# Kernel optimization log

Hardware: AMD Instinct MI355X
Metric: run time of the kernel (lower is better)

The kernel has to match this reference:

```python
import jax, jax.numpy as jnp
import numpy as np

B, A, T, D, H, NB, OUT = 64, 128, 6, 256, 512, 5, 401
ALPHA = 0.5
BETA = 0.5


def _lin_init(key, n_in, n_out, extra=()):
    bound = 1.0 / np.sqrt(n_in)
    kw, kb = jax.random.split(key)
    W = jax.random.uniform(kw, extra + (n_in, n_out), minval=-bound, maxval=bound, dtype=jnp.float32)
    b = jax.random.uniform(kb, extra + (n_out,), minval=-bound, maxval=bound, dtype=jnp.float32)
    return W, b


def setup_inputs() -> dict:
    key = jax.random.key(0)
    ks = jax.random.split(key, 8)
    stdv = 1.0 / np.sqrt(D)
    anchor = jax.random.uniform(ks[0], (1, 1, T, D), minval=-stdv, maxval=stdv, dtype=jnp.float32)
    sW1, sb1 = _lin_init(ks[1], D, D, (NB,))
    sW2, sb2 = _lin_init(ks[2], D, D, (NB,))
    cW1, cb1 = _lin_init(ks[3], D, D, (NB,))
    cW2, cb2 = _lin_init(ks[4], D, D, (NB,))
    dW1, db1 = _lin_init(ks[5], D, H)
    dW2, db2 = _lin_init(ks[6], H, OUT)
    final_embedding = jax.random.normal(ks[7], (B, A, D), dtype=jnp.float32)
    return {"final_embedding": final_embedding, "anchor": anchor,
            "sW1": sW1, "sb1": sb1, "sW2": sW2, "sb2": sb2,
            "cW1": cW1, "cb1": cb1, "cW2": cW2, "cb2": cb2,
            "dW1": dW1, "db1": db1, "dW2": dW2, "db2": db2}


def _mlp2(x, W1, b1, W2, b2):
    # 2-layer MLP (Linear -> ReLU -> Linear), applied to last dim
    return jax.nn.relu(x @ W1 + b1) @ W2 + b2


def reference(final_embedding, anchor, sW1, sb1, sW2, sb2, cW1, cb1, cW2, cb2, dW1, db1, dW2, db2):
    b, a = final_embedding.shape[:2]
    # s: [B, A, T, D] repeated anchors; c: [B, A, 1, D] context
    s = jnp.broadcast_to(anchor, (b, a, T, D))
    c = final_embedding[:, :, None, :]
    for i in range(NB):
        s_new = _mlp2(s, sW1[i], sb1[i], sW2[i], sb2[i])
        c_new = _mlp2(c, cW1[i], cb1[i], cW2[i], cb2[i])
        s_new = s_new * c_new                      # gate, broadcasts over T
        agg_c = jnp.max(s_new, axis=-2, keepdims=True)
        s = ALPHA * s + BETA * s_new               # sliding running mean
        c = ALPHA * c + BETA * agg_c
    # decoder MLP on trajectory embeddings s: [B, A, T, D]
    res = jax.nn.relu(s @ dW1 + db1) @ dW2 + db2   # [B, A, T, 401]
    coordinates = res[..., :160].reshape(b, a, T, 80, 2)
    av = res[..., 160:240].reshape(b, a, T, 80, 1)
    bv = res[..., 240:320].reshape(b, a, T, 80, 1)
    cv = res[..., 320:400].reshape(b, a, T, 80, 1)
    probas = res[..., -1]                          # [B, A, T]
    cov = jnp.concatenate([jnp.exp(av) * jnp.cosh(bv), jnp.sinh(bv),
                           jnp.sinh(bv), jnp.exp(-av) * jnp.cosh(bv)], axis=-1) * jnp.exp(cv)
    covariance_matrices = cov.reshape(b, a, T, 80, 2, 2)
    return (probas, coordinates, covariance_matrices)
```

## Files before the change

kernel.cpp:

```cpp
#include <hip/hip_runtime.h>
#include <math.h>


constexpr int Tn  = 6;
constexpr int Dn  = 256;
constexpr int Hn  = 512;
constexpr int NBn = 5;
constexpr int OUTn = 401;
constexpr int BA  = 8192;
constexpr int MR  = 49152;
constexpr float kAlpha = 0.5f;
constexpr float kBeta  = 0.5f;

typedef __bf16 bf16_8 __attribute__((ext_vector_type(8)));
typedef float  f32x4  __attribute__((ext_vector_type(4)));

__device__ __forceinline__ void async_copy16(const __bf16* g, __bf16* l) {
  __builtin_amdgcn_global_load_lds(
      (const __attribute__((address_space(1))) void*)g,
      (__attribute__((address_space(3))) void*)l, 16, 0, 0);
}

template<bool RELU, bool OUT_BF16>
__global__ __launch_bounds__(256) void gemm_mfma(
    const __bf16* __restrict__ A, const __bf16* __restrict__ BT,
    const float* __restrict__ bias, void* __restrict__ Cout,
    int M, int N, int K)
{
  __shared__ __align__(16) char smem[34816];

  const int tid = threadIdx.x;
  const int l   = tid & 63;
  const int w   = tid >> 6;
  const int wm  = w >> 1, wn = w & 1;

  const int GX = gridDim.x;
  const int total = GX * gridDim.y;
  const int L = blockIdx.y * GX + blockIdx.x;
  const int xcd = L & 7, pos = L >> 3;
  const int base = total >> 3, rem = total & 7;
  const int start = xcd * base + (xcd < rem ? xcd : rem);
  const int TL = start + pos;
  const int my = TL / GX;
  const int nx = TL - my * GX;
  const int m0 = my * 128;
  const int n0 = nx * 128;

  const int lrow = l >> 2;
  const int lk   = (l & 3) * 8;
  int ar0 = m0 + w * 32 + lrow;        if (ar0 > M - 1) ar0 = M - 1;
  int ar1 = m0 + w * 32 + 16 + lrow;   if (ar1 > M - 1) ar1 = M - 1;
  int br0 = n0 + w * 32 + lrow;        if (br0 > N - 1) br0 = N - 1;
  int br1 = n0 + w * 32 + 16 + lrow;   if (br1 > N - 1) br1 = N - 1;
  const __bf16* Ag0 = A  + (size_t)ar0 * K + lk;
  const __bf16* Ag1 = A  + (size_t)ar1 * K + lk;
  const __bf16* Bg0 = BT + (size_t)br0 * K + lk;
  const __bf16* Bg1 = BT + (size_t)br1 * K + lk;

  f32x4 acc[4][4];
#pragma unroll
  for (int i = 0; i < 4; ++i)
#pragma unroll
    for (int j = 0; j < 4; ++j) acc[i][j] = (f32x4){0.f, 0.f, 0.f, 0.f};

  auto stage = [&](int buf, int ko) {
    __bf16* As = (__bf16*)(smem + buf * 16384);
    __bf16* Bs = As + 4096;
    async_copy16(Ag0 + ko, As + w * 1024);
    async_copy16(Ag1 + ko, As + w * 1024 + 512);
    async_copy16(Bg0 + ko, Bs + w * 1024);
    async_copy16(Bg1 + ko, Bs + w * 1024 + 512);
  };

  const int kIters = K >> 5;
  stage(0, 0);
  __syncthreads();
  for (int kt = 0; kt < kIters; ++kt) {
    if (kt + 1 < kIters) stage((kt + 1) & 1, (kt + 1) * 32);
    const __bf16* As = (const __bf16*)(smem + (kt & 1) * 16384);
    const __bf16* Bs = As + 4096;
    const __bf16* ap = As + (wm * 64 + (l & 15)) * 32 + (l >> 4) * 8;
    const __bf16* bp = Bs + (wn * 64 + (l & 15)) * 32 + (l >> 4) * 8;

    bf16_8 af[4], bf[4];
#pragma unroll
    for (int i = 0; i < 4; ++i) af[i] = *(const bf16_8*)(ap + i * 16 * 32);
#pragma unroll
    for (int j = 0; j < 4; ++j) bf[j] = *(const bf16_8*)(bp + j * 16 * 32);
#pragma unroll
    for (int i = 0; i < 4; ++i)
#pragma unroll
      for (int j = 0; j < 4; ++j)
        acc[i][j] = __builtin_amdgcn_mfma_f32_16x16x32_bf16(af[i], bf[j], acc[i][j], 0, 0, 0);
    __syncthreads();
  }

  const int colb = n0 + wn * 64 + (l & 15);
  const int rowb = m0 + wm * 64 + (l >> 4) * 4;

  if (OUT_BF16) {
    __bf16* Cs = (__bf16*)smem;
    const int lrb = wm * 64 + (l >> 4) * 4;
    const int lcb = wn * 64 + (l & 15);
#pragma unroll
    for (int j = 0; j < 4; ++j) {
      const float bj = bias[colb + j * 16];
#pragma unroll
      for (int i = 0; i < 4; ++i) {
#pragma unroll
        for (int r = 0; r < 4; ++r) {
          float v = acc[i][j][r] + bj;
          if (RELU) v = fmaxf(v, 0.0f);
          Cs[(lrb + i * 16 + r) * 136 + lcb + j * 16] = (__bf16)v;
        }
      }
    }
    __syncthreads();
    __bf16* Cg = (__bf16*)Cout;
#pragma unroll
    for (int it = 0; it < 8; ++it) {
      const int idx = it * 256 + tid;
      const int row = idx >> 4, c16 = idx & 15;
      const int gr = m0 + row;
      if (gr < M) {
        uint4 v = *(const uint4*)(Cs + row * 136 + c16 * 8);
        *(uint4*)(Cg + (size_t)gr * N + n0 + c16 * 8) = v;
      }
    }
  } else {
#pragma unroll
    for (int j = 0; j < 4; ++j) {
      const int gc = colb + j * 16;
      if (gc >= N) continue;
      const float bj = bias[gc];
#pragma unroll
      for (int i = 0; i < 4; ++i) {
        const int gr0 = rowb + i * 16;
#pragma unroll
        for (int r = 0; r < 4; ++r) {
          const int gr = gr0 + r;
          if (gr >= M) continue;
          float v = acc[i][j][r] + bj;
          if (RELU) v = fmaxf(v, 0.0f);
          ((float*)Cout)[(size_t)gr * N + gc] = v;
        }
      }
    }
  }
}

__global__ __launch_bounds__(512) void mlp2_c(
    const __bf16* __restrict__ X, const __bf16* __restrict__ W1T,
    const float* __restrict__ b1, const __bf16* __restrict__ W2T,
    const float* __restrict__ b2, __bf16* __restrict__ Out)
{
  __shared__ __align__(16) char smem[53248];
  __bf16* Hb = (__bf16*)(smem + 36864);

  const int tid = threadIdx.x, l = tid & 63, w = tid >> 6;
  const int m0 = blockIdx.x * 32;
  const int q4 = (l >> 4) * 4;

  f32x4 acc[2][2];
#pragma unroll
  for (int i = 0; i < 2; ++i)
#pragma unroll
    for (int j = 0; j < 2; ++j) acc[i][j] = (f32x4){0.f, 0.f, 0.f, 0.f};

  const __bf16* Xg = X + (size_t)(m0 + (tid >> 2)) * Dn + (tid & 3) * 8;

  auto stageA = [&](int buf, int kt) {
    if (tid < 128)
      async_copy16(Xg + kt * 32, (__bf16*)(smem + buf * 2048) + tid * 8);
  };
  auto stageW = [&](const __bf16* WT, int buf, int kt) {
    __bf16* Wstb = (__bf16*)(smem + 4096 + buf * 16384);
#pragma unroll
    for (int r2 = 0; r2 < 2; ++r2) {
      const int ch = tid + r2 * 512, row = ch >> 2, kk = (ch & 3) * 8;
      async_copy16(WT + (size_t)row * Dn + kt * 32 + kk, Wstb + ch * 8);
    }
  };

  stageA(0, 0); stageW(W1T, 0, 0);
  __syncthreads();
  for (int kt = 0; kt < 8; ++kt) {
    if (kt < 7) { stageA((kt + 1) & 1, kt + 1); stageW(W1T, (kt + 1) & 1, kt + 1); }
    const __bf16* Astb = (const __bf16*)(smem + (kt & 1) * 2048);
    const __bf16* Wstb = (const __bf16*)(smem + 4096 + (kt & 1) * 16384);
    bf16_8 bf[2];
#pragma unroll
    for (int j = 0; j < 2; ++j)
      bf[j] = *(const bf16_8*)(Wstb + (w * 32 + j * 16 + (l & 15)) * 32 + (l >> 4) * 8);
#pragma unroll
    for (int i = 0; i < 2; ++i) {
      bf16_8 af = *(const bf16_8*)(Astb + (i * 16 + (l & 15)) * 32 + (l >> 4) * 8);
#pragma unroll
      for (int j = 0; j < 2; ++j)
        acc[i][j] = __builtin_amdgcn_mfma_f32_16x16x32_bf16(af, bf[j], acc[i][j], 0, 0, 0);
    }
    __syncthreads();
  }

#pragma unroll
  for (int j = 0; j < 2; ++j) {
    const int col = w * 32 + j * 16 + (l & 15);
    const float bj = b1[col];
    __bf16* hc = Hb + (col >> 5) * 1024 + (col & 31);
#pragma unroll
    for (int i = 0; i < 2; ++i)
#pragma unroll
      for (int r = 0; r < 4; ++r) {
        const int row = i * 16 + q4 + r;
        hc[row * 32] = (__bf16)fmaxf(acc[i][j][r] + bj, 0.0f);
      }
  }
  __syncthreads();

#pragma unroll
  for (int i = 0; i < 2; ++i)
#pragma unroll
    for (int j = 0; j < 2; ++j) acc[i][j] = (f32x4){0.f, 0.f, 0.f, 0.f};
  stageW(W2T, 0, 0);
  __syncthreads();
  for (int kt = 0; kt < 8; ++kt) {
    if (kt < 7) stageW(W2T, (kt + 1) & 1, kt + 1);
    const __bf16* Wstb = (const __bf16*)(smem + 4096 + (kt & 1) * 16384);
    bf16_8 bf[2];
#pragma unroll
    for (int j = 0; j < 2; ++j)
      bf[j] = *(const bf16_8*)(Wstb + (w * 32 + j * 16 + (l & 15)) * 32 + (l >> 4) * 8);
#pragma unroll
    for (int i = 0; i < 2; ++i) {
      bf16_8 af = *(const bf16_8*)(Hb + kt * 1024 + (i * 16 + (l & 15)) * 32 + (l >> 4) * 8);
#pragma unroll
      for (int j = 0; j < 2; ++j)
        acc[i][j] = __builtin_amdgcn_mfma_f32_16x16x32_bf16(af, bf[j], acc[i][j], 0, 0, 0);
    }
    __syncthreads();
  }

#pragma unroll
  for (int j = 0; j < 2; ++j) {
    const int col = w * 32 + j * 16 + (l & 15);
    const float bj = b2[col];
#pragma unroll
    for (int i = 0; i < 2; ++i)
#pragma unroll
      for (int r = 0; r < 4; ++r) {
        const int row = i * 16 + q4 + r;
        Out[(size_t)(m0 + row) * Dn + col] = (__bf16)(acc[i][j][r] + bj);
      }
  }
}

__global__ __launch_bounds__(512) void mlp2_s(
    __bf16* __restrict__ S, const __bf16* __restrict__ W1T,
    const float* __restrict__ b1, const __bf16* __restrict__ W2T,
    const float* __restrict__ b2, const __bf16* __restrict__ Cnew,
    __bf16* __restrict__ C)
{
  __shared__ __align__(16) char smem[71680];
  __bf16* Hb   = (__bf16*)(smem + 22528);
  __bf16* Snew = (__bf16*)smem;

  const int tid = threadIdx.x, l = tid & 63, w = tid >> 6;
  const int m0 = blockIdx.x * 96;
  const int q4 = (l >> 4) * 4;

  f32x4 acc[6][2];
#pragma unroll
  for (int i = 0; i < 6; ++i)
#pragma unroll
    for (int j = 0; j < 2; ++j) acc[i][j] = (f32x4){0.f, 0.f, 0.f, 0.f};

  const __bf16* Sg = S + (size_t)(m0 + (tid >> 2)) * Dn + (tid & 3) * 8;

  auto stageL1 = [&](int buf, int kt) {
    __bf16* Astb = (__bf16*)(smem + buf * 22528);
    __bf16* Wstb = (__bf16*)(smem + buf * 22528 + 6144);
    if (tid < 384) async_copy16(Sg + kt * 32, Astb + tid * 8);
#pragma unroll
    for (int r2 = 0; r2 < 2; ++r2) {
      const int ch = tid + r2 * 512, row = ch >> 2, kk = (ch & 3) * 8;
      async_copy16(W1T + (size_t)row * Dn + kt * 32 + kk, Wstb + ch * 8);
    }
  };

  stageL1(0, 0);
  __syncthreads();
  for (int kt = 0; kt < 8; ++kt) {
    if (kt < 7) stageL1((kt + 1) & 1, kt + 1);
    const __bf16* Astb = (const __bf16*)(smem + (kt & 1) * 22528);
    const __bf16* Wstb = Astb + 3072;
    bf16_8 bf[2];
#pragma unroll
    for (int j = 0; j < 2; ++j)
      bf[j] = *(const bf16_8*)(Wstb + (w * 32 + j * 16 + (l & 15)) * 32 + (l >> 4) * 8);
#pragma unroll
    for (int i = 0; i < 6; ++i) {
      bf16_8 af = *(const bf16_8*)(Astb + (i * 16 + (l & 15)) * 32 + (l >> 4) * 8);
#pragma unroll
      for (int j = 0; j < 2; ++j)
        acc[i][j] = __builtin_amdgcn_mfma_f32_16x16x32_bf16(af, bf[j], acc[i][j], 0, 0, 0);
    }
    __syncthreads();
  }

#pragma unroll
  for (int j = 0; j < 2; ++j) {
    const int col = w * 32 + j * 16 + (l & 15);
    const float bj = b1[col];
    __bf16* hc = Hb + (col >> 5) * (96 * 32) + (col & 31);
#pragma unroll
    for (int i = 0; i < 6; ++i)
#pragma unroll
      for (int r = 0; r < 4; ++r) {
        const int row = i * 16 + q4 + r;
        hc[row * 32] = (__bf16)fmaxf(acc[i][j][r] + bj, 0.0f);
      }
  }
  __syncthreads();

#pragma unroll
  for (int i = 0; i < 6; ++i)
#pragma unroll
    for (int j = 0; j < 2; ++j) acc[i][j] = (f32x4){0.f, 0.f, 0.f, 0.f};
  __bf16* Wst = (__bf16*)(smem + 6144);
  for (int kt = 0; kt < 8; ++kt) {
#pragma unroll
    for (int r2 = 0; r2 < 2; ++r2) {
      const int ch = tid + r2 * 512, row = ch >> 2, kk = (ch & 3) * 8;
      async_copy16(W2T + (size_t)row * Dn + kt * 32 + kk, Wst + ch * 8);
    }
    __syncthreads();
    bf16_8 bf[2];
#pragma unroll
    for (int j = 0; j < 2; ++j)
      bf[j] = *(const bf16_8*)(Wst + (w * 32 + j * 16 + (l & 15)) * 32 + (l >> 4) * 8);
#pragma unroll
    for (int i = 0; i < 6; ++i) {
      bf16_8 af = *(const bf16_8*)(Hb + kt * (96 * 32) + (i * 16 + (l & 15)) * 32 + (l >> 4) * 8);
#pragma unroll
      for (int j = 0; j < 2; ++j)
        acc[i][j] = __builtin_amdgcn_mfma_f32_16x16x32_bf16(af, bf[j], acc[i][j], 0, 0, 0);
    }
    __syncthreads();
  }

#pragma unroll
  for (int j = 0; j < 2; ++j) {
    const int col = w * 32 + j * 16 + (l & 15);
    const float bj = b2[col];
#pragma unroll
    for (int i = 0; i < 6; ++i)
#pragma unroll
      for (int r = 0; r < 4; ++r) {
        const int row = i * 16 + q4 + r;
        Snew[row * 264 + col] = (__bf16)(acc[i][j][r] + bj);
      }
  }
  __syncthreads();

  {
    const int ba = tid >> 5, dg = (tid & 31) * 8;
    const size_t gb = (size_t)(blockIdx.x * 16 + ba) * Dn + dg;
    bf16_8 cn8 = *(const bf16_8*)(Cnew + gb);
    float cn[8], m[8];
#pragma unroll
    for (int e = 0; e < 8; ++e) { cn[e] = (float)cn8[e]; m[e] = -3.402823466e38f; }
#pragma unroll
    for (int t = 0; t < Tn; ++t) {
      const int row = ba * 6 + t;
      bf16_8 sn8 = *(const bf16_8*)(Snew + row * 264 + dg);
      const size_t gs = (size_t)(m0 + row) * Dn + dg;
      bf16_8 s8 = *(const bf16_8*)(S + gs);
      bf16_8 o8;
#pragma unroll
      for (int e = 0; e < 8; ++e) {
        const float sn = (float)sn8[e] * cn[e];
        m[e] = fmaxf(m[e], sn);
        o8[e] = (__bf16)(kAlpha * (float)s8[e] + kBeta * sn);
      }
      *(bf16_8*)(S + gs) = o8;
    }
    bf16_8 c8 = *(const bf16_8*)(C + gb);
#pragma unroll
    for (int e = 0; e < 8; ++e)
      c8[e] = (__bf16)(kAlpha * (float)c8[e] + kBeta * m[e]);
    *(bf16_8*)(C + gb) = c8;
  }
}

__global__ __launch_bounds__(512, 4) void decoder2_fused(
    const __bf16* __restrict__ A, const __bf16* __restrict__ BT,
    const float* __restrict__ bias, float* __restrict__ out)
{
  __shared__ __align__(16) char smem[73728];
  float* mid = (float*)smem;

  const int tid = threadIdx.x, l = tid & 63, w = tid >> 6;
  const int m0 = blockIdx.x * 64;
  const int q4 = (l >> 4) * 4;

  f32x4 acc[4][4];
#pragma unroll
  for (int i = 0; i < 4; ++i)
#pragma unroll
    for (int j = 0; j < 4; ++j) acc[i][j] = (f32x4){0.f, 0.f, 0.f, 0.f};

  const __bf16* Ag = A + (size_t)(m0 + (tid >> 2)) * Hn + (tid & 3) * 8;
  const __bf16* Bg[4];
#pragma unroll
  for (int r4 = 0; r4 < 4; ++r4) {
    const int ch = tid + r4 * 512;
    int row = ch >> 2; if (row > 400) row = 400;
    Bg[r4] = BT + (size_t)row * Hn + (ch & 3) * 8;
  }

  auto stage = [&](int buf, int kt) {
    const int ko = kt * 32;
    __bf16* base = (__bf16*)(smem + buf * 36864);
    if (tid < 256) async_copy16(Ag + ko, base + tid * 8);
    __bf16* Bl = base + 64 * 32;
#pragma unroll
    for (int r4 = 0; r4 < 4; ++r4)
      async_copy16(Bg[r4] + ko, Bl + (size_t)(tid + r4 * 512) * 8);
  };

  stage(0, 0);
  __syncthreads();
  int cur = 0;
  for (int kt = 0; kt < 16; ++kt) {
    if (kt < 15) stage(cur ^ 1, kt + 1);
    const __bf16* Asl = (const __bf16*)(smem + cur * 36864);
    const __bf16* Bsl = Asl + 64 * 32;
    bf16_8 af[4], bf[4];
#pragma unroll
    for (int j = 0; j < 4; ++j)
      bf[j] = *(const bf16_8*)(Bsl + (w * 64 + j * 16 + (l & 15)) * 32 + (l >> 4) * 8);
#pragma unroll
    for (int i = 0; i < 4; ++i)
      af[i] = *(const bf16_8*)(Asl + (i * 16 + (l & 15)) * 32 + (l >> 4) * 8);
#pragma unroll
    for (int i = 0; i < 4; ++i)
#pragma unroll
      for (int j = 0; j < 4; ++j)
        acc[i][j] = __builtin_amdgcn_mfma_f32_16x16x32_bf16(af[i], bf[j], acc[i][j], 0, 0, 0);
    __syncthreads();
    cur ^= 1;
  }

  float* cov = out + MR + (size_t)MR * 160;
  const int gc = w * 64 + (l & 15);
#pragma unroll
  for (int sub = 0; sub < 2; ++sub) {
#pragma unroll
    for (int ih = 0; ih < 2; ++ih) {
      const int i = sub * 2 + ih;
#pragma unroll
      for (int j = 0; j < 4; ++j) {
        const int c = gc + j * 16;
        if (c > 400) continue;
        const float bj = bias[c];
#pragma unroll
        for (int r = 0; r < 4; ++r) {
          const int lr = ih * 16 + q4 + r;
          const int gr = m0 + sub * 32 + lr;
          const float v = acc[i][j][r] + bj;
          if (c < 160)      out[(size_t)MR + (size_t)gr * 160 + c] = v;
          else if (c < 400) mid[lr * 241 + (c - 160)] = v;
          else              out[gr] = v;
        }
      }
    }
    __syncthreads();
#pragma unroll
    for (int p = 0; p < 5; ++p) {
      const int q = p * 512 + tid;
      const int r32 = q / 80, j = q - r32 * 80;
      const int gr = m0 + sub * 32 + r32;
      const float av = mid[r32 * 241 + j];
      const float bv = mid[r32 * 241 + 80 + j];
      const float cv = mid[r32 * 241 + 160 + j];
      const float eb = __expf(bv), ebn = __expf(-bv);
      const float sh = 0.5f * (eb - ebn), ch = 0.5f * (eb + ebn);
      const float ea = __expf(av), ean = __expf(-av), ec = __expf(cv);
      f32x4 c4 = { ea * ch * ec, sh * ec, sh * ec, ean * ch * ec };
      *(f32x4*)(cov + (size_t)gr * 320 + 4 * j) = c4;
    }
    if (sub == 0) __syncthreads();
  }
}

__global__ __launch_bounds__(256) void transpose_bf16(
    const float* __restrict__ W, __bf16* __restrict__ WT, int K, int N)
{
  __shared__ float t[32][33];
  const int b  = blockIdx.z;
  const int tx = threadIdx.x, ty = threadIdx.y;
  const int k0 = blockIdx.y * 32, n0 = blockIdx.x * 32;
  const float* Wb  = W  + (size_t)b * K * N;
  __bf16*      WTb = WT + (size_t)b * N * K;
#pragma unroll
  for (int r = 0; r < 4; ++r) {
    int kk = k0 + ty + r * 8;
    if (kk < K && n0 + tx < N) t[ty + r * 8][tx] = Wb[(size_t)kk * N + n0 + tx];
  }
  __syncthreads();
#pragma unroll
  for (int r = 0; r < 4; ++r) {
    int nn = n0 + ty + r * 8;
    if (nn < N && k0 + tx < K)
      WTb[(size_t)nn * K + k0 + tx] = (__bf16)t[tx][ty + r * 8];
  }
}

__global__ __launch_bounds__(256) void convert_bf16(
    const float* __restrict__ in, __bf16* __restrict__ out, int n)
{
  int i = blockIdx.x * 256 + threadIdx.x;
  if (i < n) out[i] = (__bf16)in[i];
}

__global__ __launch_bounds__(256) void ew_update0(
    const float* __restrict__ anchor, const float* __restrict__ fe,
    const float* __restrict__ snewsm, const __bf16* __restrict__ cnew,
    __bf16* __restrict__ s, __bf16* __restrict__ c)
{
  int q = blockIdx.x * 256 + threadIdx.x;
  if (q >= BA * 32) return;
  int ba = q >> 5;
  int dg = (q & 31) * 8;
  bf16_8 cn8 = *(const bf16_8*)(cnew + (size_t)ba * Dn + dg);
  float cn[8], m[8];
#pragma unroll
  for (int e = 0; e < 8; ++e) { cn[e] = (float)cn8[e]; m[e] = -3.402823466e38f; }
  size_t base = (size_t)ba * Tn * Dn + dg;
#pragma unroll
  for (int t = 0; t < Tn; ++t) {
    bf16_8 o8;
#pragma unroll
    for (int e = 0; e < 8; ++e) {
      float sn = snewsm[t * Dn + dg + e] * cn[e];
      m[e] = fmaxf(m[e], sn);
      o8[e] = (__bf16)(kAlpha * anchor[t * Dn + dg + e] + kBeta * sn);
    }
    *(bf16_8*)(s + base + t * Dn) = o8;
  }
  bf16_8 c8;
#pragma unroll
  for (int e = 0; e < 8; ++e)
    c8[e] = (__bf16)(kAlpha * fe[(size_t)ba * Dn + dg + e] + kBeta * m[e]);
  *(bf16_8*)(c + (size_t)ba * Dn + dg) = c8;
}

extern "C" void kernel_launch(void* const* d_in, const int* in_sizes, int n_in,
                              void* d_out, int out_size, void* d_ws, size_t ws_size,
                              hipStream_t stream) {
  const float* fe     = (const float*)d_in[0];
  const float* anchor = (const float*)d_in[1];
  const float* sW1 = (const float*)d_in[2];
  const float* sb1 = (const float*)d_in[3];
  const float* sW2 = (const float*)d_in[4];
  const float* sb2 = (const float*)d_in[5];
  const float* cW1 = (const float*)d_in[6];
  const float* cb1 = (const float*)d_in[7];
  const float* cW2 = (const float*)d_in[8];
  const float* cb2 = (const float*)d_in[9];
  const float* dW1 = (const float*)d_in[10];
  const float* db1 = (const float*)d_in[11];
  const float* dW2 = (const float*)d_in[12];
  const float* db2 = (const float*)d_in[13];
  float* out = (float*)d_out;

  char* p = (char*)d_ws;
  __bf16* s_bf    = (__bf16*)(p + 0);
  __bf16* hd_bf   = (__bf16*)(p + 25165824);
  __bf16* c_bf    = (__bf16*)(p + 75497472);
  __bf16* cnew_bf = (__bf16*)(p + 79691776);
  __bf16* fe_bf   = (__bf16*)(p + 83886080);
  __bf16* sWT1    = (__bf16*)(p + 88080384);
  __bf16* sWT2    = (__bf16*)(p + 88735744);
  __bf16* cWT1    = (__bf16*)(p + 89391104);
  __bf16* cWT2    = (__bf16*)(p + 90046464);
  __bf16* dWT1    = (__bf16*)(p + 90701824);
  __bf16* dWT2    = (__bf16*)(p + 90963968);
  __bf16* anc_bf  = (__bf16*)(p + 91374592);
  __bf16* hsm_bf  = (__bf16*)(p + 91377664);
  float*  snewsm_f= (float* )(p + 91380736);

  auto gemm = [&](const __bf16* A, const __bf16* BT, const float* b, void* C,
                  int M, int N, int K, bool relu, bool outbf) {
    dim3 grid((N + 127) / 128, (M + 127) / 128);
    if (relu) {
      if (outbf) gemm_mfma<true,  true ><<<grid, 256, 0, stream>>>(A, BT, b, C, M, N, K);
      else       gemm_mfma<true,  false><<<grid, 256, 0, stream>>>(A, BT, b, C, M, N, K);
    } else {
      if (outbf) gemm_mfma<false, true ><<<grid, 256, 0, stream>>>(A, BT, b, C, M, N, K);
      else       gemm_mfma<false, false><<<grid, 256, 0, stream>>>(A, BT, b, C, M, N, K);
    }
  };

  {
    dim3 blk(32, 8);
    dim3 g88(8, 8, NBn);
    transpose_bf16<<<g88, blk, 0, stream>>>(sW1, sWT1, Dn, Dn);
    transpose_bf16<<<g88, blk, 0, stream>>>(sW2, sWT2, Dn, Dn);
    transpose_bf16<<<g88, blk, 0, stream>>>(cW1, cWT1, Dn, Dn);
    transpose_bf16<<<g88, blk, 0, stream>>>(cW2, cWT2, Dn, Dn);
    transpose_bf16<<<dim3(16, 8, 1), blk, 0, stream>>>(dW1, dWT1, Dn, Hn);
    transpose_bf16<<<dim3(13, 16, 1), blk, 0, stream>>>(dW2, dWT2, Hn, OUTn);
  }
  convert_bf16<<<(BA * Dn + 255) / 256, 256, 0, stream>>>(fe, fe_bf, BA * Dn);
  convert_bf16<<<(Tn * Dn + 255) / 256, 256, 0, stream>>>(anchor, anc_bf, Tn * Dn);

  const size_t WKK = (size_t)Dn * Dn;

  gemm(anc_bf, sWT1, sb1, hsm_bf,   Tn, Dn, Dn, true,  true);
  gemm(hsm_bf, sWT2, sb2, snewsm_f, Tn, Dn, Dn, false, false);
  mlp2_c<<<BA / 32, 512, 0, stream>>>(fe_bf, cWT1, cb1, cWT2, cb2, cnew_bf);
  ew_update0<<<(BA * 32 + 255) / 256, 256, 0, stream>>>(anchor, fe, snewsm_f,
                                                        cnew_bf, s_bf, c_bf);

  for (int i = 1; i < NBn; ++i) {
    mlp2_c<<<BA / 32, 512, 0, stream>>>(c_bf, cWT1 + i * WKK, cb1 + i * Dn,
                                        cWT2 + i * WKK, cb2 + i * Dn, cnew_bf);
    mlp2_s<<<MR / 96, 512, 0, stream>>>(s_bf, sWT1 + i * WKK, sb1 + i * Dn,
                                        sWT2 + i * WKK, sb2 + i * Dn,
                                        cnew_bf, c_bf);
  }

  gemm(s_bf, dWT1, db1, hd_bf, MR, Hn, Dn, true, true);
  decoder2_fused<<<MR / 64, 512, 0, stream>>>(hd_bf, dWT2, db2, out);
}
```

Measured before the change: 393.4 us.

## Fuse context MLP into trajectory MLP kernel per block

Merges the separate mlp2_c launch into mlp2_s, so each block first computes the context MLP for its own 16 agent rows and keeps the result in shared memory. This removes one kernel launch per block iteration and the global round trip for c_new. In exchange, each block does a serial 16-row MLP with poor MFMA utilisation (one A tile per step) before its main work, which lengthens the critical path inside each block.

Result: faster. 374.4 us (-4.8%).

```diff
diff --git a/kernel.cpp b/kernel.cpp
--- a/kernel.cpp
+++ b/kernel.cpp
@@ -254,19 +254,108 @@
   }
 }
 
-__global__ __launch_bounds__(512) void mlp2_s(
-    __bf16* __restrict__ S, const __bf16* __restrict__ W1T,
-    const float* __restrict__ b1, const __bf16* __restrict__ W2T,
-    const float* __restrict__ b2, const __bf16* __restrict__ Cnew,
+__global__ __launch_bounds__(512) void mlp2_cs(
+    __bf16* __restrict__ S,
+    const __bf16* __restrict__ sW1T, const float* __restrict__ sb1,
+    const __bf16* __restrict__ sW2T, const float* __restrict__ sb2,
+    const __bf16* __restrict__ cW1T, const float* __restrict__ cb1,
+    const __bf16* __restrict__ cW2T, const float* __restrict__ cb2,
     __bf16* __restrict__ C)
 {
   __shared__ __align__(16) char smem[71680];
-  __bf16* Hb   = (__bf16*)(smem + 22528);
-  __bf16* Snew = (__bf16*)smem;
+  __bf16* Hb    = (__bf16*)(smem + 22528);
+  __bf16* Snew  = (__bf16*)smem;
+  __bf16* Hc    = (__bf16*)(smem + 45056);
+  __bf16* CnewL = (__bf16*)(smem + 53248);
 
   const int tid = threadIdx.x, l = tid & 63, w = tid >> 6;
-  const int m0 = blockIdx.x * 96;
-  const int q4 = (l >> 4) * 4;
+  const int m0  = blockIdx.x * 96;
+  const int ba0 = blockIdx.x * 16;
+  const int q4  = (l >> 4) * 4;
+
+  {
+    f32x4 ac[2];
+    ac[0] = (f32x4){0.f, 0.f, 0.f, 0.f};
+    ac[1] = (f32x4){0.f, 0.f, 0.f, 0.f};
+
+    const __bf16* Cg = C + (size_t)(ba0 + (tid >> 2)) * Dn + (tid & 3) * 8;
+
+    auto stageC1 = [&](int buf, int kt) {
+      __bf16* Astb = (__bf16*)(smem + buf * 22528);
+      __bf16* Wstb = Astb + 3072;
+      if (tid < 64) async_copy16(Cg + kt * 32, Astb + tid * 8);
+#pragma unroll
+      for (int r2 = 0; r2 < 2; ++r2) {
+        const int ch = tid + r2 * 512, row = ch >> 2, kk = (ch & 3) * 8;
+        async_copy16(cW1T + (size_t)row * Dn + kt * 32 + kk, Wstb + ch * 8);
+      }
+    };
+    stageC1(0, 0);
+    __syncthreads();
+    for (int kt = 0; kt < 8; ++kt) {
+      if (kt < 7) stageC1((kt + 1) & 1, kt + 1);
+      const __bf16* Astb = (const __bf16*)(smem + (kt & 1) * 22528);
+      const __bf16* Wstb = Astb + 3072;
+      bf16_8 bf[2];
+#pragma unroll
+      for (int j = 0; j < 2; ++j)
+        bf[j] = *(const bf16_8*)(Wstb + (w * 32 + j * 16 + (l & 15)) * 32 + (l >> 4) * 8);
+      bf16_8 af = *(const bf16_8*)(Astb + (l & 15) * 32 + (l >> 4) * 8);
+#pragma unroll
+      for (int j = 0; j < 2; ++j)
+        ac[j] = __builtin_amdgcn_mfma_f32_16x16x32_bf16(af, bf[j], ac[j], 0, 0, 0);
+      __syncthreads();
+    }
+
+#pragma unroll
+    for (int j = 0; j < 2; ++j) {
+      const int col = w * 32 + j * 16 + (l & 15);
+      const float bj = cb1[col];
+      __bf16* hc = Hc + (col >> 5) * 512 + (col & 31);
+#pragma unroll
+      for (int r = 0; r < 4; ++r)
+        hc[(q4 + r) * 32] = (__bf16)fmaxf(ac[j][r] + bj, 0.0f);
+    }
+    __syncthreads();
+
+    ac[0] = (f32x4){0.f, 0.f, 0.f, 0.f};
+    ac[1] = (f32x4){0.f, 0.f, 0.f, 0.f};
+    auto stageC2 = [&](int buf, int kt) {
+      __bf16* Wstb = (__bf16*)(smem + buf * 22528 + 6144);
+#pragma unroll
+      for (int r2 = 0; r2 < 2; ++r2) {
+        const int ch = tid + r2 * 512, row = ch >> 2, kk = (ch & 3) * 8;
+        async_copy16(cW2T + (size_t)row * Dn + kt * 32 + kk, Wstb + ch * 8);
+      }
+    };
+    stageC2(0, 0);
+    __syncthreads();
+    for (int kt = 0; kt < 8; ++kt) {
+      if (kt < 7) stageC2((kt + 1) & 1, kt + 1);
+      const __bf16* Wstb = (const __bf16*)(smem + (kt & 1) * 22528 + 6144);
+      bf16_8 bf[2];
+#pragma unroll
+      for (int j = 0; j < 2; ++j)
+        bf[j] = *(const bf16_8*)(Wstb + (w * 32 + j * 16 + (l & 15)) * 32 + (l >> 4) * 8);
+      bf16_8 af = *(const bf16_8*)(Hc + kt * 512 + (l & 15) * 32 + (l >> 4) * 8);
+#pragma unroll
+      for (int j = 0; j < 2; ++j)
+        ac[j] = __builtin_amdgcn_mfma_f32_16x16x32_bf16(af, bf[j], ac[j], 0, 0, 0);
+      __syncthreads();
+    }
+
+#pragma unroll
+    for (int j = 0; j < 2; ++j) {
+      const int col = w * 32 + j * 16 + (l & 15);
+      const float bj = cb2[col];
+#pragma unroll
+      for (int r = 0; r < 4; ++r)
+        CnewL[(q4 + r) * 264 + col] = (__bf16)(ac[j][r] + bj);
+    }
+    __syncthreads();
+  }
+
+  bf16_8 cn8 = *(const bf16_8*)(CnewL + (tid >> 5) * 264 + (tid & 31) * 8);
 
   f32x4 acc[6][2];
 #pragma unroll
@@ -283,7 +372,7 @@
 #pragma unroll
     for (int r2 = 0; r2 < 2; ++r2) {
       const int ch = tid + r2 * 512, row = ch >> 2, kk = (ch & 3) * 8;
-      async_copy16(W1T + (size_t)row * Dn + kt * 32 + kk, Wstb + ch * 8);
+      async_copy16(sW1T + (size_t)row * Dn + kt * 32 + kk, Wstb + ch * 8);
     }
   };
 
@@ -310,7 +399,7 @@
 #pragma unroll
   for (int j = 0; j < 2; ++j) {
     const int col = w * 32 + j * 16 + (l & 15);
-    const float bj = b1[col];
+    const float bj = sb1[col];
     __bf16* hc = Hb + (col >> 5) * (96 * 32) + (col & 31);
 #pragma unroll
     for (int i = 0; i < 6; ++i)
@@ -331,7 +420,7 @@
 #pragma unroll
     for (int r2 = 0; r2 < 2; ++r2) {
       const int ch = tid + r2 * 512, row = ch >> 2, kk = (ch & 3) * 8;
-      async_copy16(W2T + (size_t)row * Dn + kt * 32 + kk, Wst + ch * 8);
+      async_copy16(sW2T + (size_t)row * Dn + kt * 32 + kk, Wst + ch * 8);
     }
     __syncthreads();
     bf16_8 bf[2];
@@ -351,7 +440,7 @@
 #pragma unroll
   for (int j = 0; j < 2; ++j) {
     const int col = w * 32 + j * 16 + (l & 15);
-    const float bj = b2[col];
+    const float bj = sb2[col];
 #pragma unroll
     for (int i = 0; i < 6; ++i)
 #pragma unroll
@@ -364,8 +453,7 @@
 
   {
     const int ba = tid >> 5, dg = (tid & 31) * 8;
-    const size_t gb = (size_t)(blockIdx.x * 16 + ba) * Dn + dg;
-    bf16_8 cn8 = *(const bf16_8*)(Cnew + gb);
+    const size_t gb = (size_t)(ba0 + ba) * Dn + dg;
     float cn[8], m[8];
 #pragma unroll
     for (int e = 0; e < 8; ++e) { cn[e] = (float)cn8[e]; m[e] = -3.402823466e38f; }
@@ -624,11 +712,11 @@
                                                         cnew_bf, s_bf, c_bf);
 
   for (int i = 1; i < NBn; ++i) {
-    mlp2_c<<<BA / 32, 512, 0, stream>>>(c_bf, cWT1 + i * WKK, cb1 + i * Dn,
-                                        cWT2 + i * WKK, cb2 + i * Dn, cnew_bf);
-    mlp2_s<<<MR / 96, 512, 0, stream>>>(s_bf, sWT1 + i * WKK, sb1 + i * Dn,
-                                        sWT2 + i * WKK, sb2 + i * Dn,
-                                        cnew_bf, c_bf);
+    mlp2_cs<<<MR / 96, 512, 0, stream>>>(
+        s_bf,
+        sWT1 + i * WKK, sb1 + i * Dn, sWT2 + i * WKK, sb2 + i * Dn,
+        cWT1 + i * WKK, cb1 + i * Dn, cWT2 + i * WKK, cb2 + i * Dn,
+        c_bf);
   }
 
   gemm(s_bf, dWT1, db1, hd_bf, MR, Hn, Dn, true, true);
```
